# Kernel optimization log

Measured on AMD Instinct MI355X. Metric: run time of the kernel, lower is better.

The kernel has to match this reference:

```python
import jax, jax.numpy as jnp
import numpy as np

N, D_IN, D_OUT, E, H = 2048, 1024, 256, 50, 256  # tokens, input_dim, output_dim, edge_nodes, expert hidden
RH = 512  # distributed_processor hidden


def setup_inputs() -> dict:
    key = jax.random.key(0)
    ks = jax.random.split(key, 16)
    w = lambda k, shape: jax.random.normal(k, shape, jnp.float32) * 0.02
    z = lambda *shape: jnp.zeros(shape, jnp.float32)
    return {
        "x": jax.random.normal(ks[0], (N, D_IN), jnp.float32),
        # 50 expert MLPs: Linear(D_IN,H)-ReLU-Linear(H,D_OUT), stacked over E
        "ew1": w(ks[1], (E, D_IN, H)), "eb1": z(E, H),
        "ew2": w(ks[2], (E, H, D_OUT)), "eb2": z(E, D_OUT),
        # distributed_processor: Linear(E*D_OUT,RH)-ReLU-Linear(RH,D_OUT)
        "dw1": w(ks[3], (E * D_OUT, RH)), "db1": z(RH),
        "dw2": w(ks[4], (RH, D_OUT)), "db2": z(D_OUT),
        # latency_optimizer: Linear(D_IN,256)-ReLU-Linear(256,1)-Sigmoid
        "lw1": w(ks[5], (D_IN, 256)), "lb1": z(256),
        "lw2": w(ks[6], (256, 1)), "lb2": z(1),
        # bandwidth_optimizer: same structure
        "bw1": w(ks[7], (D_IN, 256)), "bb1": z(256),
        "bw2": w(ks[8], (256, 1)), "bb2": z(1),
        # privacy_preserver: Linear(D_OUT,256)-ReLU-Linear(256,D_OUT)
        "pw1": w(ks[9], (D_OUT, 256)), "pb1": z(256),
        "pw2": w(ks[10], (256, D_OUT)), "pb2": z(D_OUT),
    }


def reference(x, ew1, eb1, ew2, eb2, dw1, db1, dw2, db2,
              lw1, lb1, lw2, lb2, bw1, bb1, bw2, bb2,
              pw1, pb1, pw2, pb2):
    n = x.shape[0]
    # grouped expert MLPs (replaces the Python for-loop over edge nodes)
    h = jax.nn.relu(jnp.einsum('ni,eih->neh', x, ew1) + eb1)        # [N,E,H]
    expert_out = jnp.einsum('neh,eho->neo', h, ew2) + eb2           # [N,E,D_OUT]
    cat = expert_out.reshape(n, E * D_OUT)                          # torch.cat(dim=-1)
    # distributed_processor reduce
    dist = jax.nn.relu(cat @ dw1 + db1) @ dw2 + db2                 # [N,D_OUT]
    # gating scalars
    lat = jax.nn.sigmoid(jax.nn.relu(x @ lw1 + lb1) @ lw2 + lb2)    # [N,1]
    bwd = jax.nn.sigmoid(jax.nn.relu(x @ bw1 + bb1) @ bw2 + bb2)    # [N,1]
    # privacy_preserver
    priv = jax.nn.relu(dist @ pw1 + pb1) @ pw2 + pb2                # [N,D_OUT]
    return priv * lat * bwd
```

## Files before the change

kernel.cpp:

```cpp
#include <hip/hip_runtime.h>
#include <hip/hip_bf16.h>

typedef unsigned short u16;
typedef __attribute__((ext_vector_type(8))) __bf16 v8bf;
typedef __attribute__((ext_vector_type(4))) float v4f;

#define DEVINL __device__ __forceinline__

DEVINL u16 f2bf(float f) {
  union { float f; unsigned u; } v; v.f = f;
  unsigned u = v.u;
  return (u16)((u + 0x7FFFu + ((u >> 16) & 1u)) >> 16);
}
DEVINL float bf2f(u16 b) {
  union { unsigned u; float f; } v; v.u = ((unsigned)b) << 16;
  return v.f;
}

DEVINL void async16(const void* g, void* l) {
  __builtin_amdgcn_global_load_lds(
      (__attribute__((address_space(1))) void*)(g),
      (__attribute__((address_space(3))) void*)(l), 16, 0, 0);
}

DEVINL void f2b_body(const float* __restrict__ src, u16* __restrict__ dst, int base) {
  int i = base + threadIdx.x * 4;
  float4 v = *(const float4*)(src + i);
  unsigned lo = (unsigned)f2bf(v.x) | ((unsigned)f2bf(v.y) << 16);
  unsigned hi = (unsigned)f2bf(v.z) | ((unsigned)f2bf(v.w) << 16);
  uint2 o; o.x = lo; o.y = hi;
  *(uint2*)(dst + i) = o;
}

DEVINL void tr64(u16 (*t)[66], const float* __restrict__ src,
                 u16* __restrict__ dst, int R, int C, int bx, int by) {
  int r0 = by * 64, c0 = bx * 64;
  int tx = threadIdx.x & 15, ty = threadIdx.x >> 4;
#pragma unroll
  for (int i = 0; i < 4; ++i) {
    int rr = ty + i * 16;
    float4 v = *(const float4*)(src + (long)(r0 + rr) * C + c0 + tx * 4);
    u16* d = &t[rr][tx * 4];
    d[0] = f2bf(v.x); d[1] = f2bf(v.y); d[2] = f2bf(v.z); d[3] = f2bf(v.w);
  }
  __syncthreads();
#pragma unroll
  for (int i = 0; i < 4; ++i) {
    int cc = ty + i * 16;
    ushort4 o;
    o.x = t[tx * 4 + 0][cc]; o.y = t[tx * 4 + 1][cc];
    o.z = t[tx * 4 + 2][cc]; o.w = t[tx * 4 + 3][cc];
    *(ushort4*)(dst + (long)(c0 + cc) * R + r0 + tx * 4) = o;
  }
}

__global__ __launch_bounds__(256) void k_prep(
    const float* __restrict__ x, const float* __restrict__ ew2,
    const float* __restrict__ ew1, const float* __restrict__ dw1,
    const float* __restrict__ dw2, const float* __restrict__ lw1,
    const float* __restrict__ bw1, const float* __restrict__ pw1,
    const float* __restrict__ pw2,
    const float* __restrict__ eb1, const float* __restrict__ lb1,
    const float* __restrict__ bb1,
    u16* __restrict__ xb, u16* __restrict__ ew2b, u16* __restrict__ ew1tf,
    u16* __restrict__ dw1t, u16* __restrict__ dw2t,
    u16* __restrict__ pw1t, u16* __restrict__ pw2t,
    float* __restrict__ ebcat) {
  __shared__ u16 tile[64][66];
  int b = blockIdx.x;
  if (b < 2048) { f2b_body(x, xb, b * 1024); return; }
  b -= 2048;
  if (b < 3200) { f2b_body(ew2, ew2b, b * 1024); return; }
  b -= 3200;
  if (b < 3200) {
    int e = b >> 6, t = b & 63;
    tr64(tile, ew1 + (long)e * 1024 * 256, ew1tf + (long)e * 256 * 1024,
         1024, 256, t & 3, t >> 2);
    return;
  }
  b -= 3200;
  if (b < 1600) {
    tr64(tile, dw1, dw1t, 12800, 512, b & 7, b >> 3);
    return;
  }
  b -= 1600;
  if (b < 32) {
    tr64(tile, dw2, dw2t, 512, 256, b & 3, b >> 2);
    return;
  }
  b -= 32;
  if (b < 64) {
    tr64(tile, lw1, ew1tf + (long)12800 * 1024, 1024, 256, b & 3, b >> 2);
    return;
  }
  b -= 64;
  if (b < 64) {
    tr64(tile, bw1, ew1tf + (long)13056 * 1024, 1024, 256, b & 3, b >> 2);
    return;
  }
  b -= 64;
  if (b < 16) {
    tr64(tile, pw1, pw1t, 256, 256, b & 3, b >> 2);
    return;
  }
  b -= 16;
  if (b < 16) {
    tr64(tile, pw2, pw2t, 256, 256, b & 3, b >> 2);
    return;
  }
  b -= 16;
  {
    int i = b * 256 + threadIdx.x;
    float v;
    if (i < 12800) v = eb1[i];
    else if (i < 13056) v = lb1[i - 12800];
    else v = bb1[i - 13056];
    ebcat[i] = v;
  }
}

DEVINL void gemm128_body(u16* __restrict__ sA, u16* __restrict__ sB,
    int bx, int by, int z,
    const u16* __restrict__ A, int lda, long aBatch,
    const u16* __restrict__ B, int ldb, long bBatch,
    void* __restrict__ Cp, int ldc, long cBatch,
    int K,
    const float* __restrict__ bias, long biasBatch,
    const float* __restrict__ rowscale, int flags) {
  const int tid = threadIdx.x;
  const int w = tid >> 6, l = tid & 63;
  const u16* Ab = A + (long)z * aBatch + (long)by * 128 * lda;
  const u16* Bb = B + (long)z * bBatch + (long)bx * 128 * ldb;
  const int ldaB = lda * 2, ldbB = ldb * 2;
  const int wm = w >> 1, wn = w & 1;
  const int r = l & 15, kq = l >> 4;

  const int f0 = w * 1024 + l * 16;
  const int f1 = f0 + 4096;
  const int row0 = f0 >> 6, cb0 = f0 & 63;
  const int row1 = f1 >> 6, cb1 = f1 & 63;
  const int seg0 = w * 1024, seg1 = seg0 + 4096;

  v4f acc[4][4];
#pragma unroll
  for (int m = 0; m < 4; ++m)
#pragma unroll
    for (int n = 0; n < 4; ++n) acc[m][n] = v4f{0.f, 0.f, 0.f, 0.f};

  const char* gA = (const char*)Ab;
  const char* gB = (const char*)Bb;
  const int nkt = K / 32;

  async16(gA + (long)row0 * ldaB + cb0, (char*)sA + seg0);
  async16(gA + (long)row1 * ldaB + cb1, (char*)sA + seg1);
  async16(gB + (long)row0 * ldbB + cb0, (char*)sB + seg0);
  async16(gB + (long)row1 * ldbB + cb1, (char*)sB + seg1);
  __syncthreads();

  for (int kt = 0; kt < nkt; ++kt) {
    const int cur = kt & 1;
    if (kt + 1 < nkt) {
      const long ko = (long)(kt + 1) * 64;
      async16(gA + ko + (long)row0 * ldaB + cb0, (char*)sA + (cur ^ 1) * 8192 + seg0);
      async16(gA + ko + (long)row1 * ldaB + cb1, (char*)sA + (cur ^ 1) * 8192 + seg1);
      async16(gB + ko + (long)row0 * ldbB + cb0, (char*)sB + (cur ^ 1) * 8192 + seg0);
      async16(gB + ko + (long)row1 * ldbB + cb1, (char*)sB + (cur ^ 1) * 8192 + seg1);
    }
    v8bf af[4], bfr[4];
#pragma unroll
    for (int m = 0; m < 4; ++m)
      af[m] = *(const v8bf*)&sA[cur * 4096 + (wm * 64 + m * 16 + r) * 32 + kq * 8];
#pragma unroll
    for (int n = 0; n < 4; ++n)
      bfr[n] = *(const v8bf*)&sB[cur * 4096 + (wn * 64 + n * 16 + r) * 32 + kq * 8];
#pragma unroll
    for (int m = 0; m < 4; ++m)
#pragma unroll
      for (int n = 0; n < 4; ++n)
        acc[m][n] = __builtin_amdgcn_mfma_f32_16x16x32_bf16(af[m], bfr[n], acc[m][n], 0, 0, 0);
    __syncthreads();
  }

  const float* bz = bias ? (bias + (long)z * biasBatch) : nullptr;
  const long rowBase = (long)by * 128 + wm * 64 + kq * 4;
  const int colBase = bx * 128 + wn * 64 + r;
  float* Cf = (float*)Cp + (long)z * cBatch;
  u16* Ch = (u16*)Cp + (long)z * cBatch;
#pragma unroll
  for (int m = 0; m < 4; ++m) {
#pragma unroll
    for (int n = 0; n < 4; ++n) {
      const int col = colBase + n * 16;
      const float bv = bz ? bz[col] : 0.f;
#pragma unroll
      for (int i = 0; i < 4; ++i) {
        const long row = rowBase + m * 16 + i;
        float v = acc[m][n][i] + bv;
        if (flags & 1) v = fmaxf(v, 0.f);
        if (rowscale) v *= rowscale[row];
        const long idx = row * ldc + col;
        if (flags & 2) Cf[idx] = v;
        else Ch[idx] = f2bf(v);
      }
    }
  }
}

__global__ __launch_bounds__(256) void k_gemm(
    const u16* __restrict__ A, int lda, long aBatch,
    const u16* __restrict__ B, int ldb, long bBatch,
    void* __restrict__ Cp, int ldc, long cBatch,
    int K,
    const float* __restrict__ bias, long biasBatch,
    const float* __restrict__ rowscale, int flags) {
  __shared__ __align__(16) u16 sA[2 * 4096];
  __shared__ __align__(16) u16 sB[2 * 4096];
  gemm128_body(sA, sB, blockIdx.x, blockIdx.y, blockIdx.z,
               A, lda, aBatch, B, ldb, bBatch, Cp, ldc, cBatch, K,
               bias, biasBatch, rowscale, flags);
}

__global__ __launch_bounds__(256) void k_wft_bias(
    const u16* __restrict__ dw1t, const u16* __restrict__ ew2b,
    u16* __restrict__ Wft,
    const float* __restrict__ eb2, const float* __restrict__ db1,
    float* __restrict__ biasf) {
  __shared__ __align__(16) u16 sA[2 * 4096];
  __shared__ __align__(16) u16 sB[2 * 4096];
  int b = blockIdx.x;
  if (b < 512) {
    const u16* row = dw1t + (long)b * 12800;
    float s = 0.f;
    for (int c = threadIdx.x; c < 1600; c += 256) {
      ushort4 a0 = *(const ushort4*)(row + c * 8);
      ushort4 a1 = *(const ushort4*)(row + c * 8 + 4);
      float4 e0 = *(const float4*)(eb2 + c * 8);
      float4 e1 = *(const float4*)(eb2 + c * 8 + 4);
      s += bf2f(a0.x) * e0.x + bf2f(a0.y) * e0.y + bf2f(a0.z) * e0.z + bf2f(a0.w) * e0.w
         + bf2f(a1.x) * e1.x + bf2f(a1.y) * e1.y + bf2f(a1.z) * e1.z + bf2f(a1.w) * e1.w;
    }
    float* red = (float*)sA;
    red[threadIdx.x] = s;
    __syncthreads();
    for (int off = 128; off > 0; off >>= 1) {
      if (threadIdx.x < off) red[threadIdx.x] += red[threadIdx.x + off];
      __syncthreads();
    }
    if (threadIdx.x == 0) biasf[b] = red[0] + db1[b];
    return;
  }
  b -= 512;
  int bx = b & 1, by = (b >> 1) & 3, z = b >> 3;
  gemm128_body(sA, sB, bx, by, z,
               dw1t, 12800, 256, ew2b, 256, (long)256 * 256,
               Wft, 12800, 256, 256, nullptr, 0, nullptr, 0);
}

#define LDS_T(buf, op) (smem + ((buf) * 2 + (op)) * 16384)

#define READ_A(buf, mh) do {                                                   \
  const char* _t = (const char*)LDS_T(buf, 0);                                 \
  _Pragma("unroll") for (int m = 0; m < 4; ++m)                                \
    _Pragma("unroll") for (int kk = 0; kk < 2; ++kk)                           \
      a[m][kk] = *(const v8bf*)(_t +                                           \
        (wm * 128 + (mh) * 64 + m * 16 + r15) * 128 +                          \
        ((kk * 64 + kq * 16) ^ (swr << 4)));                                   \
} while (0)

#define READ_B(buf, nh, br) do {                                               \
  const char* _t = (const char*)LDS_T(buf, 1);                                 \
  _Pragma("unroll") for (int n = 0; n < 2; ++n)                                \
    _Pragma("unroll") for (int kk = 0; kk < 2; ++kk)                           \
      br[n][kk] = *(const v8bf*)(_t +                                          \
        (wn * 64 + (nh) * 32 + n * 16 + r15) * 128 +                          \
        ((kk * 64 + kq * 16) ^ (swr << 4)));                                   \
} while (0)

#define MMA(mh, nh, br) do {                                                   \
  _Pragma("unroll") for (int kk = 0; kk < 2; ++kk)                             \
    _Pragma("unroll") for (int m = 0; m < 4; ++m)                              \
      _Pragma("unroll") for (int n = 0; n < 2; ++n)                            \
        acc[(mh) * 4 + m][(nh) * 2 + n] =                                      \
          __builtin_amdgcn_mfma_f32_16x16x32_bf16(                             \
            a[m][kk], br[n][kk], acc[(mh) * 4 + m][(nh) * 2 + n], 0, 0, 0);    \
} while (0)

#define BAR() __builtin_amdgcn_s_barrier()
#define PRIO1() __builtin_amdgcn_s_setprio(1)
#define PRIO0() __builtin_amdgcn_s_setprio(0)
#define VM6() asm volatile("s_waitcnt vmcnt(6)" ::: "memory")
#define VM0() asm volatile("s_waitcnt vmcnt(0)" ::: "memory")

__global__ __launch_bounds__(512, 2) void k_gemm256(
    const u16* __restrict__ A, int lda, long aBatch,
    const u16* __restrict__ B, int ldb, long bBatch,
    void* __restrict__ Cp, int ldc, long cBatch,
    int K, int NX,
    const float* __restrict__ bias,
    const float* __restrict__ rowscale, int flags) {
  __shared__ __align__(16) u16 smem[2 * 2 * 16384];

  const int lin = blockIdx.x;
  const int idx = (lin & 7) * NX + (lin >> 3);
  const int by = idx & 7, bx = idx >> 3;

  const int tid = threadIdx.x;
  const int w = tid >> 6, l = tid & 63;
  const int wm = w >> 2, wn = w & 3;
  const int r15 = l & 15, kq = l >> 4, swr = l & 7;
  const int z = blockIdx.z;

  const int rl = l >> 3;
  const int scol = ((l & 7) ^ rl) << 4;

  const long ldaB = (long)lda * 2, ldbB = (long)ldb * 2;
  const char* gAs = (const char*)(A + (long)z * aBatch) +
                    ((long)by * 256 + rl) * ldaB + scol;
  const char* gBs = (const char*)(B + (long)z * bBatch) +
                    ((long)bx * 256 + rl) * ldbB + scol;

  auto stA = [&](int buf, int R0, int kt) {
    async16(gAs + (long)R0 * ldaB + (long)kt * 128, (char*)LDS_T(buf, 0) + R0 * 128);
  };
  auto stB = [&](int buf, int R0, int kt) {
    async16(gBs + (long)R0 * ldbB + (long)kt * 128, (char*)LDS_T(buf, 1) + R0 * 128);
  };
  auto stAU0 = [&](int buf, int kt) { stA(buf, w * 8, kt);       stA(buf, 128 + w * 8, kt); };
  auto stAU1 = [&](int buf, int kt) { stA(buf, 64 + w * 8, kt);  stA(buf, 192 + w * 8, kt); };
  auto stBU0 = [&](int buf, int kt) { int R = (w >> 1) * 64 + (w & 1) * 16;      stB(buf, R, kt); stB(buf, R + 8, kt); };
  auto stBU1 = [&](int buf, int kt) { int R = (w >> 1) * 64 + (w & 1) * 16 + 32; stB(buf, R, kt); stB(buf, R + 8, kt); };

  v4f acc[8][4];
#pragma unroll
  for (int m = 0; m < 8; ++m)
#pragma unroll
    for (int n = 0; n < 4; ++n) acc[m][n] = v4f{0.f, 0.f, 0.f, 0.f};
  v8bf a[4][2], b0[2][2], b1[2][2];

  const int NT = K >> 6;
  const int NI = (NT >> 1) - 1;

  stAU0(0, 0); stBU0(0, 0); stBU1(0, 0); stAU1(0, 0);
  stAU0(1, 1); stBU0(1, 1); stBU1(1, 1);
  VM6();
  BAR();

  int kt0 = 0;
  for (int i = 0; i < NI; ++i, kt0 += 2) {
    READ_A(0, 0); READ_B(0, 0, b0);
    stAU1(1, kt0 + 1);
    BAR(); PRIO1(); MMA(0, 0, b0); PRIO0(); BAR();
    READ_B(0, 1, b1);
    stAU0(0, kt0 + 2);
    BAR(); PRIO1(); MMA(0, 1, b1); PRIO0(); BAR();
    READ_A(0, 1);
    stBU0(0, kt0 + 2);
    BAR(); PRIO1(); MMA(1, 1, b1); PRIO0(); BAR();
    stBU1(0, kt0 + 2);
    BAR(); PRIO1(); MMA(1, 0, b0); PRIO0(); VM6(); BAR();
    READ_A(1, 0); READ_B(1, 0, b0);
    stAU1(0, kt0 + 2);
    BAR(); PRIO1(); MMA(0, 0, b0); PRIO0(); BAR();
    READ_B(1, 1, b1);
    stAU0(1, kt0 + 3);
    BAR(); PRIO1(); MMA(0, 1, b1); PRIO0(); BAR();
    READ_A(1, 1);
    stBU0(1, kt0 + 3);
    BAR(); PRIO1(); MMA(1, 1, b1); PRIO0(); BAR();
    stBU1(1, kt0 + 3);
    BAR(); PRIO1(); MMA(1, 0, b0); PRIO0(); VM6(); BAR();
  }

  READ_A(0, 0); READ_B(0, 0, b0);
  stAU1(1, kt0 + 1);
  BAR(); PRIO1(); MMA(0, 0, b0); PRIO0(); BAR();
  READ_B(0, 1, b1);
  BAR(); PRIO1(); MMA(0, 1, b1); PRIO0(); BAR();
  READ_A(0, 1);
  BAR(); PRIO1(); MMA(1, 1, b1); PRIO0(); BAR();
  BAR(); PRIO1(); MMA(1, 0, b0); PRIO0(); VM0(); BAR();
  READ_A(1, 0); READ_B(1, 0, b0);
  BAR(); PRIO1(); MMA(0, 0, b0); PRIO0(); BAR();
  READ_B(1, 1, b1);
  BAR(); PRIO1(); MMA(0, 1, b1); PRIO0(); BAR();
  READ_A(1, 1);
  BAR(); PRIO1(); MMA(1, 1, b1); PRIO0(); BAR();
  PRIO1(); MMA(1, 0, b0); PRIO0();

  const long rowBase = (long)by * 256 + wm * 128 + kq * 4;
  const int colBase = bx * 256 + wn * 64 + r15;
  float* Cf = (float*)Cp + (long)z * cBatch;
  u16* Ch = (u16*)Cp + (long)z * cBatch;
#pragma unroll
  for (int mf = 0; mf < 8; ++mf) {
#pragma unroll
    for (int nf = 0; nf < 4; ++nf) {
      const int col = colBase + nf * 16;
      const float bv = bias ? bias[col] : 0.f;
#pragma unroll
      for (int j = 0; j < 4; ++j) {
        const long row = rowBase + mf * 16 + j;
        float v = acc[mf][nf][j] + bv;
        if (flags & 1) v = fmaxf(v, 0.f);
        if (rowscale) v *= rowscale[row];
        const long idx = row * ldc + col;
        if (flags & 2) Cf[idx] = v;
        else Ch[idx] = f2bf(v);
      }
    }
  }
}

__global__ __launch_bounds__(256) void k_splitk_reduce(
    const float* __restrict__ part, const float* __restrict__ bias,
    u16* __restrict__ dst, int total, int S, int nred,
    const u16* __restrict__ lbh, int ldl,
    const float* __restrict__ lw2, const float* __restrict__ lb2,
    const float* __restrict__ bw2, const float* __restrict__ bb2,
    float* __restrict__ g) {
  if ((int)blockIdx.x >= nred) {
    int bid = blockIdx.x - nred;
    int w = threadIdx.x >> 6, l = threadIdx.x & 63;
    int n = bid * 4 + w;
    const u16* rowp = lbh + (long)n * ldl;
    float sa = 0.f, sb = 0.f;
#pragma unroll
    for (int j = 0; j < 4; ++j) {
      int i = l * 4 + j;
      sa += bf2f(rowp[i]) * lw2[i];
      sb += bf2f(rowp[256 + i]) * bw2[i];
    }
#pragma unroll
    for (int off = 32; off > 0; off >>= 1) {
      sa += __shfl_down(sa, off, 64);
      sb += __shfl_down(sb, off, 64);
    }
    if (l == 0) {
      float ga = 1.f / (1.f + expf(-(sa + lb2[0])));
      float gb = 1.f / (1.f + expf(-(sb + bb2[0])));
      g[n] = ga * gb;
    }
    return;
  }
  int i = blockIdx.x * 256 + threadIdx.x;
  float s = 0.f;
  for (int k = 0; k < S; ++k) s += part[(long)k * total + i];
  s += bias[i & 511];
  dst[i] = f2bf(fmaxf(s, 0.f));
}

__global__ __launch_bounds__(256) void k_tail(
    const u16* __restrict__ dh,
    const u16* __restrict__ dw2t,
    const float* __restrict__ db2,
    const u16* __restrict__ pw1t,
    const float* __restrict__ pb1,
    const u16* __restrict__ pw2t,
    const float* __restrict__ pb2,
    const float* __restrict__ g,
    float* __restrict__ out) {
  __shared__ __align__(16) u16 dhs[16][520];
  __shared__ __align__(16) u16 ds2[16][264];
  __shared__ __align__(16) u16 phs[16][264];
  const int tid = threadIdx.x;
  const int w = tid >> 6, l = tid & 63;
  const int r = l & 15, kq = l >> 4;
  const int r0 = blockIdx.x * 16;

#pragma unroll
  for (int i = 0; i < 4; ++i) {
    int e = (tid + i * 256) * 8;
    int row = e >> 9, col = e & 511;
    *(v8bf*)&dhs[row][col] = *(const v8bf*)(dh + (long)(r0 + row) * 512 + col);
  }
  __syncthreads();

  v4f acc[4];
#pragma unroll
  for (int n = 0; n < 4; ++n) acc[n] = v4f{0.f, 0.f, 0.f, 0.f};
#pragma unroll 4
  for (int kt = 0; kt < 16; ++kt) {
    v8bf af = *(const v8bf*)&dhs[r][kt * 32 + kq * 8];
#pragma unroll
    for (int n = 0; n < 4; ++n) {
      v8bf bf = *(const v8bf*)(dw2t + (long)(w * 64 + n * 16 + r) * 512 + kt * 32 + kq * 8);
      acc[n] = __builtin_amdgcn_mfma_f32_16x16x32_bf16(af, bf, acc[n], 0, 0, 0);
    }
  }
#pragma unroll
  for (int n = 0; n < 4; ++n) {
    int col = w * 64 + n * 16 + r;
    float bv = db2[col];
#pragma unroll
    for (int j = 0; j < 4; ++j) ds2[kq * 4 + j][col] = f2bf(acc[n][j] + bv);
  }
  __syncthreads();

#pragma unroll
  for (int n = 0; n < 4; ++n) acc[n] = v4f{0.f, 0.f, 0.f, 0.f};
#pragma unroll 4
  for (int kt = 0; kt < 8; ++kt) {
    v8bf af = *(const v8bf*)&ds2[r][kt * 32 + kq * 8];
#pragma unroll
    for (int n = 0; n < 4; ++n) {
      v8bf bf = *(const v8bf*)(pw1t + (long)(w * 64 + n * 16 + r) * 256 + kt * 32 + kq * 8);
      acc[n] = __builtin_amdgcn_mfma_f32_16x16x32_bf16(af, bf, acc[n], 0, 0, 0);
    }
  }
#pragma unroll
  for (int n = 0; n < 4; ++n) {
    int col = w * 64 + n * 16 + r;
    float bv = pb1[col];
#pragma unroll
    for (int j = 0; j < 4; ++j) phs[kq * 4 + j][col] = f2bf(fmaxf(acc[n][j] + bv, 0.f));
  }
  __syncthreads();

#pragma unroll
  for (int n = 0; n < 4; ++n) acc[n] = v4f{0.f, 0.f, 0.f, 0.f};
#pragma unroll 4
  for (int kt = 0; kt < 8; ++kt) {
    v8bf af = *(const v8bf*)&phs[r][kt * 32 + kq * 8];
#pragma unroll
    for (int n = 0; n < 4; ++n) {
      v8bf bf = *(const v8bf*)(pw2t + (long)(w * 64 + n * 16 + r) * 256 + kt * 32 + kq * 8);
      acc[n] = __builtin_amdgcn_mfma_f32_16x16x32_bf16(af, bf, acc[n], 0, 0, 0);
    }
  }
#pragma unroll
  for (int n = 0; n < 4; ++n) {
    int col = w * 64 + n * 16 + r;
    float bv = pb2[col];
#pragma unroll
    for (int j = 0; j < 4; ++j) {
      int row = kq * 4 + j;
      out[(long)(r0 + row) * 256 + col] = (acc[n][j] + bv) * g[r0 + row];
    }
  }
}

extern "C" void kernel_launch(void* const* d_in, const int* in_sizes, int n_in,
                              void* d_out, int out_size, void* d_ws, size_t ws_size,
                              hipStream_t stream) {
  const float* x   = (const float*)d_in[0];
  const float* ew1 = (const float*)d_in[1];
  const float* eb1 = (const float*)d_in[2];
  const float* ew2 = (const float*)d_in[3];
  const float* eb2 = (const float*)d_in[4];
  const float* dw1 = (const float*)d_in[5];
  const float* db1 = (const float*)d_in[6];
  const float* dw2 = (const float*)d_in[7];
  const float* db2 = (const float*)d_in[8];
  const float* lw1 = (const float*)d_in[9];
  const float* lb1 = (const float*)d_in[10];
  const float* lw2 = (const float*)d_in[11];
  const float* lb2 = (const float*)d_in[12];
  const float* bw1 = (const float*)d_in[13];
  const float* bb1 = (const float*)d_in[14];
  const float* bw2 = (const float*)d_in[15];
  const float* bb2 = (const float*)d_in[16];
  const float* pw1 = (const float*)d_in[17];
  const float* pb1 = (const float*)d_in[18];
  const float* pw2 = (const float*)d_in[19];
  const float* pb2 = (const float*)d_in[20];

  const int S = 8, Ksplit = 1600;

  char* p = (char*)d_ws;
  auto alloc = [&](size_t bytes) {
    char* q = p;
    p += (bytes + 255) & ~(size_t)255;
    return q;
  };
  u16* xb      = (u16*)alloc((size_t)2048 * 1024 * 2);
  u16* ew1tf   = (u16*)alloc((size_t)13312 * 1024 * 2);
  u16* Wft     = (u16*)alloc((size_t)512 * 12800 * 2);
  u16* dw2t    = (u16*)alloc((size_t)256 * 512 * 2);
  u16* pw1t    = (u16*)alloc((size_t)256 * 256 * 2);
  u16* pw2t    = (u16*)alloc((size_t)256 * 256 * 2);
  float* ebcat = (float*)alloc(13312 * 4);
  float* biasf = (float*)alloc(512 * 4);
  u16* dh      = (u16*)alloc((size_t)2048 * 512 * 2);
  float* g     = (float*)alloc(2048 * 4);
  float* part  = (float*)alloc((size_t)S * 2048 * 512 * 4);
  char* uni    = alloc((size_t)2048 * 13312 * 2);
  u16* h_all   = (u16*)uni;
  u16* ew2b    = (u16*)uni;
  u16* dw1t    = (u16*)(uni + (((size_t)50 * 256 * 256 * 2 + 255) & ~(size_t)255));
  (void)in_sizes; (void)n_in; (void)out_size; (void)ws_size;

  k_prep<<<dim3(10292), 256, 0, stream>>>(
      x, ew2, ew1, dw1, dw2, lw1, bw1, pw1, pw2, eb1, lb1, bb1,
      xb, ew2b, ew1tf, dw1t, dw2t, pw1t, pw2t, ebcat);

  k_wft_bias<<<dim3(912), 256, 0, stream>>>(dw1t, ew2b, Wft, eb2, db1, biasf);

  k_gemm256<<<dim3(416, 1, 1), 512, 0, stream>>>(
      xb, 1024, 0, ew1tf, 1024, 0, h_all, 13312, 0,
      1024, 52, ebcat, nullptr, 1);

  k_gemm<<<dim3(4, 16, S), 256, 0, stream>>>(
      h_all, 13312, Ksplit, Wft, 12800, Ksplit, part, 512, (long)2048 * 512,
      Ksplit, nullptr, 0, nullptr, 2);

  k_splitk_reduce<<<dim3(4608), 256, 0, stream>>>(
      part, biasf, dh, 2048 * 512, S, 4096,
      h_all + 12800, 13312, lw2, lb2, bw2, bb2, g);

  k_tail<<<dim3(128), 256, 0, stream>>>(
      dh, dw2t, db2, pw1t, pb1, pw2t, pb2, g, (float*)d_out);
}
```

Measured before the change: 193.9 us.

## Fuse split-K reduction and gating into tail kernel; add LDS waits before MMA

```diff
diff --git a/kernel.cpp b/kernel.cpp
--- a/kernel.cpp
+++ b/kernel.cpp
@@ -290,6 +290,7 @@
 #define PRIO0() __builtin_amdgcn_s_setprio(0)
 #define VM6() asm volatile("s_waitcnt vmcnt(6)" ::: "memory")
 #define VM0() asm volatile("s_waitcnt vmcnt(0)" ::: "memory")
+#define LGKM0() asm volatile("s_waitcnt lgkmcnt(0)" ::: "memory")
 
 __global__ __launch_bounds__(512, 2) void k_gemm256(
     const u16* __restrict__ A, int lda, long aBatch,
@@ -349,42 +350,42 @@
   for (int i = 0; i < NI; ++i, kt0 += 2) {
     READ_A(0, 0); READ_B(0, 0, b0);
     stAU1(1, kt0 + 1);
-    BAR(); PRIO1(); MMA(0, 0, b0); PRIO0(); BAR();
+    BAR(); LGKM0(); PRIO1(); MMA(0, 0, b0); PRIO0(); BAR();
     READ_B(0, 1, b1);
     stAU0(0, kt0 + 2);
-    BAR(); PRIO1(); MMA(0, 1, b1); PRIO0(); BAR();
+    BAR(); LGKM0(); PRIO1(); MMA(0, 1, b1); PRIO0(); BAR();
     READ_A(0, 1);
     stBU0(0, kt0 + 2);
-    BAR(); PRIO1(); MMA(1, 1, b1); PRIO0(); BAR();
+    BAR(); LGKM0(); PRIO1(); MMA(1, 1, b1); PRIO0(); BAR();
     stBU1(0, kt0 + 2);
     BAR(); PRIO1(); MMA(1, 0, b0); PRIO0(); VM6(); BAR();
     READ_A(1, 0); READ_B(1, 0, b0);
     stAU1(0, kt0 + 2);
-    BAR(); PRIO1(); MMA(0, 0, b0); PRIO0(); BAR();
+    BAR(); LGKM0(); PRIO1(); MMA(0, 0, b0); PRIO0(); BAR();
     READ_B(1, 1, b1);
     stAU0(1, kt0 + 3);
-    BAR(); PRIO1(); MMA(0, 1, b1); PRIO0(); BAR();
+    BAR(); LGKM0(); PRIO1(); MMA(0, 1, b1); PRIO0(); BAR();
     READ_A(1, 1);
     stBU0(1, kt0 + 3);
-    BAR(); PRIO1(); MMA(1, 1, b1); PRIO0(); BAR();
+    BAR(); LGKM0(); PRIO1(); MMA(1, 1, b1); PRIO0(); BAR();
     stBU1(1, kt0 + 3);
     BAR(); PRIO1(); MMA(1, 0, b0); PRIO0(); VM6(); BAR();
   }
 
   READ_A(0, 0); READ_B(0, 0, b0);
   stAU1(1, kt0 + 1);
-  BAR(); PRIO1(); MMA(0, 0, b0); PRIO0(); BAR();
+  BAR(); LGKM0(); PRIO1(); MMA(0, 0, b0); PRIO0(); BAR();
   READ_B(0, 1, b1);
-  BAR(); PRIO1(); MMA(0, 1, b1); PRIO0(); BAR();
+  BAR(); LGKM0(); PRIO1(); MMA(0, 1, b1); PRIO0(); BAR();
   READ_A(0, 1);
-  BAR(); PRIO1(); MMA(1, 1, b1); PRIO0(); BAR();
+  BAR(); LGKM0(); PRIO1(); MMA(1, 1, b1); PRIO0(); BAR();
   BAR(); PRIO1(); MMA(1, 0, b0); PRIO0(); VM0(); BAR();
   READ_A(1, 0); READ_B(1, 0, b0);
-  BAR(); PRIO1(); MMA(0, 0, b0); PRIO0(); BAR();
+  BAR(); LGKM0(); PRIO1(); MMA(0, 0, b0); PRIO0(); BAR();
   READ_B(1, 1, b1);
-  BAR(); PRIO1(); MMA(0, 1, b1); PRIO0(); BAR();
+  BAR(); LGKM0(); PRIO1(); MMA(0, 1, b1); PRIO0(); BAR();
   READ_A(1, 1);
-  BAR(); PRIO1(); MMA(1, 1, b1); PRIO0(); BAR();
+  BAR(); LGKM0(); PRIO1(); MMA(1, 1, b1); PRIO0(); BAR();
   PRIO1(); MMA(1, 0, b0); PRIO0();
 
   const long rowBase = (long)by * 256 + wm * 128 + kq * 4;
@@ -411,67 +412,69 @@
   }
 }
 
-__global__ __launch_bounds__(256) void k_splitk_reduce(
-    const float* __restrict__ part, const float* __restrict__ bias,
-    u16* __restrict__ dst, int total, int S, int nred,
-    const u16* __restrict__ lbh, int ldl,
+__global__ __launch_bounds__(256) void k_tail(
+    const float* __restrict__ part,
+    const float* __restrict__ biasf,
+    const u16* __restrict__ hg,
     const float* __restrict__ lw2, const float* __restrict__ lb2,
     const float* __restrict__ bw2, const float* __restrict__ bb2,
-    float* __restrict__ g) {
-  if ((int)blockIdx.x >= nred) {
-    int bid = blockIdx.x - nred;
-    int w = threadIdx.x >> 6, l = threadIdx.x & 63;
-    int n = bid * 4 + w;
-    const u16* rowp = lbh + (long)n * ldl;
-    float sa = 0.f, sb = 0.f;
-#pragma unroll
-    for (int j = 0; j < 4; ++j) {
-      int i = l * 4 + j;
-      sa += bf2f(rowp[i]) * lw2[i];
-      sb += bf2f(rowp[256 + i]) * bw2[i];
-    }
-#pragma unroll
-    for (int off = 32; off > 0; off >>= 1) {
-      sa += __shfl_down(sa, off, 64);
-      sb += __shfl_down(sb, off, 64);
-    }
-    if (l == 0) {
-      float ga = 1.f / (1.f + expf(-(sa + lb2[0])));
-      float gb = 1.f / (1.f + expf(-(sb + bb2[0])));
-      g[n] = ga * gb;
-    }
-    return;
-  }
-  int i = blockIdx.x * 256 + threadIdx.x;
-  float s = 0.f;
-  for (int k = 0; k < S; ++k) s += part[(long)k * total + i];
-  s += bias[i & 511];
-  dst[i] = f2bf(fmaxf(s, 0.f));
-}
-
-__global__ __launch_bounds__(256) void k_tail(
-    const u16* __restrict__ dh,
     const u16* __restrict__ dw2t,
     const float* __restrict__ db2,
     const u16* __restrict__ pw1t,
     const float* __restrict__ pb1,
     const u16* __restrict__ pw2t,
     const float* __restrict__ pb2,
-    const float* __restrict__ g,
     float* __restrict__ out) {
   __shared__ __align__(16) u16 dhs[16][520];
   __shared__ __align__(16) u16 ds2[16][264];
   __shared__ __align__(16) u16 phs[16][264];
+  __shared__ float gl[16];
   const int tid = threadIdx.x;
   const int w = tid >> 6, l = tid & 63;
   const int r = l & 15, kq = l >> 4;
   const int r0 = blockIdx.x * 16;
 
 #pragma unroll
-  for (int i = 0; i < 4; ++i) {
-    int e = (tid + i * 256) * 8;
+  for (int i = 0; i < 8; ++i) {
+    int e = (i * 256 + tid) * 4;
     int row = e >> 9, col = e & 511;
-    *(v8bf*)&dhs[row][col] = *(const v8bf*)(dh + (long)(r0 + row) * 512 + col);
+    const float* pp = part + (long)(r0 + row) * 512 + col;
+    float4 s = *(const float4*)pp;
+#pragma unroll
+    for (int k = 1; k < 8; ++k) {
+      float4 t = *(const float4*)(pp + (long)k * (2048 * 512));
+      s.x += t.x; s.y += t.y; s.z += t.z; s.w += t.w;
+    }
+    float4 bv = *(const float4*)(biasf + col);
+    ushort4 o;
+    o.x = f2bf(fmaxf(s.x + bv.x, 0.f));
+    o.y = f2bf(fmaxf(s.y + bv.y, 0.f));
+    o.z = f2bf(fmaxf(s.z + bv.z, 0.f));
+    o.w = f2bf(fmaxf(s.w + bv.w, 0.f));
+    *(ushort4*)&dhs[row][col] = o;
+  }
+
+#pragma unroll
+  for (int j = 0; j < 4; ++j) {
+    int rr = w * 4 + j;
+    const u16* rowp = hg + (long)(r0 + rr) * 13312;
+    float sa = 0.f, sb = 0.f;
+#pragma unroll
+    for (int jj = 0; jj < 4; ++jj) {
+      int i = l * 4 + jj;
+      sa += bf2f(rowp[i]) * lw2[i];
+      sb += bf2f(rowp[256 + i]) * bw2[i];
+    }
+#pragma unroll
+    for (int off = 32; off > 0; off >>= 1) {
+      sa += __shfl_down(sa, off, 64);
+      sb += __shfl_down(sb, off, 64);
+    }
+    if (l == 0) {
+      float ga = 1.f / (1.f + expf(-(sa + lb2[0])));
+      float gb = 1.f / (1.f + expf(-(sb + bb2[0])));
+      gl[rr] = ga * gb;
+    }
   }
   __syncthreads();
 
@@ -534,7 +537,7 @@
 #pragma unroll
     for (int j = 0; j < 4; ++j) {
       int row = kq * 4 + j;
-      out[(long)(r0 + row) * 256 + col] = (acc[n][j] + bv) * g[r0 + row];
+      out[(long)(r0 + row) * 256 + col] = (acc[n][j] + bv) * gl[row];
     }
   }
 }
@@ -580,8 +583,6 @@
   u16* pw2t    = (u16*)alloc((size_t)256 * 256 * 2);
   float* ebcat = (float*)alloc(13312 * 4);
   float* biasf = (float*)alloc(512 * 4);
-  u16* dh      = (u16*)alloc((size_t)2048 * 512 * 2);
-  float* g     = (float*)alloc(2048 * 4);
   float* part  = (float*)alloc((size_t)S * 2048 * 512 * 4);
   char* uni    = alloc((size_t)2048 * 13312 * 2);
   u16* h_all   = (u16*)uni;
@@ -603,10 +604,7 @@
       h_all, 13312, Ksplit, Wft, 12800, Ksplit, part, 512, (long)2048 * 512,
       Ksplit, nullptr, 0, nullptr, 2);
 
-  k_splitk_reduce<<<dim3(4608), 256, 0, stream>>>(
-      part, biasf, dh, 2048 * 512, S, 4096,
-      h_all + 12800, 13312, lw2, lb2, bw2, bb2, g);
-
   k_tail<<<dim3(128), 256, 0, stream>>>(
-      dh, dw2t, db2, pw1t, pb1, pw2t, pb2, g, (float*)d_out);
-}
+      part, biasf, h_all + 12800, lw2, lb2, bw2, bb2,
+      dw2t, db2, pw1t, pb1, pw2t, pb2, (float*)d_out);
+}
```

Result: no change. 191.8 us (-1.1%).
